# Optimization experiments

Hardware: AMD Instinct MI355X
Metric: run time of the kernel (lower is better)

Reference implementation:

```python
import jax, jax.numpy as jnp
import numpy as np

B, S, H, L, NH, FF, V, NL = 16, 512, 768, 12, 12, 3072, 30522, 9
DH = H // NH


def setup_inputs() -> dict:
    key = jax.random.key(0)
    ks = iter(jax.random.split(key, 16))
    def w(shape, scale=0.02):
        return jax.random.normal(next(ks), shape, jnp.float32) * scale
    return {
        "input_word_ids": jax.random.randint(next(ks), (B, S), 0, V, jnp.int32),
        "input_mask": jnp.ones((B, S), jnp.int32),
        "input_type_ids": jnp.zeros((B, S), jnp.int32),
        "valid_mask": jax.random.randint(next(ks), (B, S), 0, 2, jnp.int32),
        "word_emb": w((V, H)),
        "pos_emb": w((S, H)),
        "type_emb": w((2, H)),
        "emb_ln_g": jnp.ones((H,), jnp.float32),
        "emb_ln_b": jnp.zeros((H,), jnp.float32),
        "Wq": w((L, H, H)), "bq": jnp.zeros((L, H), jnp.float32),
        "Wk": w((L, H, H)), "bk": jnp.zeros((L, H), jnp.float32),
        "Wv": w((L, H, H)), "bv": jnp.zeros((L, H), jnp.float32),
        "Wo": w((L, H, H)), "bo": jnp.zeros((L, H), jnp.float32),
        "ln1_g": jnp.ones((L, H), jnp.float32), "ln1_b": jnp.zeros((L, H), jnp.float32),
        "W1": w((L, H, FF)), "b1": jnp.zeros((L, FF), jnp.float32),
        "W2": w((L, FF, H)), "b2": jnp.zeros((L, H), jnp.float32),
        "ln2_g": jnp.ones((L, H), jnp.float32), "ln2_b": jnp.zeros((L, H), jnp.float32),
        "cls_W": w((H, NL)), "cls_b": jnp.zeros((NL,), jnp.float32),
    }


def _layer_norm(x, g, b):
    m = x.mean(-1, keepdims=True)
    v = ((x - m) ** 2).mean(-1, keepdims=True)
    return (x - m) * jax.lax.rsqrt(v + 1e-12) * g + b


def reference(input_word_ids, input_mask, input_type_ids, valid_mask,
              word_emb, pos_emb, type_emb, emb_ln_g, emb_ln_b,
              Wq, bq, Wk, bk, Wv, bv, Wo, bo, ln1_g, ln1_b,
              W1, b1, W2, b2, ln2_g, ln2_b, cls_W, cls_b):
    b, s = input_word_ids.shape
    # --- BERT embeddings ---
    x = word_emb[input_word_ids] + pos_emb[None, :s] + type_emb[input_type_ids]
    x = _layer_norm(x, emb_ln_g, emb_ln_b)  # [B,S,H]
    attn_bias = (1.0 - input_mask.astype(jnp.float32))[:, None, None, :] * -1e9
    scale = 1.0 / np.sqrt(DH).astype(np.float32)

    def step(h, p):
        wq, bq_, wk, bk_, wv, bv_, wo, bo_, g1, gb1, w1, wb1, w2, wb2, g2, gb2 = p
        q = (h @ wq + bq_).reshape(b, s, NH, DH)
        k = (h @ wk + bk_).reshape(b, s, NH, DH)
        v = (h @ wv + bv_).reshape(b, s, NH, DH)
        scores = jnp.einsum('bqhd,bkhd->bhqk', q, k) * scale + attn_bias
        probs = jax.nn.softmax(scores, axis=-1)
        ctx = jnp.einsum('bhqk,bkhd->bqhd', probs, v).reshape(b, s, H)
        h = _layer_norm(h + ctx @ wo + bo_, g1, gb1)
        ff = jax.nn.gelu(h @ w1 + wb1, approximate=False)
        h = _layer_norm(h + ff @ w2 + wb2, g2, gb2)
        return h, None

    params = (Wq, bq, Wk, bk, Wv, bv, Wo, bo, ln1_g, ln1_b, W1, b1, W2, b2, ln2_g, ln2_b)
    x, _ = jax.lax.scan(step, x, params)

    # --- valid-token compaction (vectorized form of the python double loop) ---
    # valid tokens packed to the front (stable order), remainder zero-padded
    invalid = (1 - valid_mask).astype(jnp.int32)
    perm = jnp.argsort(invalid, axis=1, stable=True)          # [B,S]
    compact = jnp.take_along_axis(x, perm[:, :, None], axis=1)
    counts = valid_mask.sum(axis=1)                           # [B]
    keep = (jnp.arange(s)[None, :] < counts[:, None])[:, :, None]
    compact = jnp.where(keep, compact, jnp.zeros((), x.dtype))
    # dropout is identity at inference (training=False)
    logits = jax.nn.softmax(compact @ cls_W + cls_b, axis=-1)  # [B,S,NL]
    return logits
```

## Files before the change

### kernel.cpp

```cpp
#include <hip/hip_runtime.h>
#include <cstdint>
#include <cstddef>

#define B_ 16
#define S_ 512
#define H_ 768
#define L_ 12
#define NH_ 12
#define DH_ 64
#define FF_ 3072
#define NL_ 9

typedef _Float16 f16x8 __attribute__((ext_vector_type(8)));
typedef float f32x4 __attribute__((ext_vector_type(4)));

__device__ __forceinline__ float block_sum256(float v, float* red) {
#pragma unroll
  for (int off = 32; off; off >>= 1) v += __shfl_down(v, off);
  __syncthreads();
  if ((threadIdx.x & 63) == 0) red[threadIdx.x >> 6] = v;
  __syncthreads();
  return red[0] + red[1] + red[2] + red[3];
}

__device__ __forceinline__ float gelu_f(float x) {
  return 0.5f * x * (1.0f + erff(x * 0.70710678118654752f));
}

__global__ __launch_bounds__(256) void embed_ln_kernel(
    const int* __restrict__ wid, const int* __restrict__ tpid,
    const float* __restrict__ we, const float* __restrict__ pe,
    const float* __restrict__ te, const float* __restrict__ g,
    const float* __restrict__ bb, float* __restrict__ h,
    _Float16* __restrict__ hb) {
  __shared__ float red[4];
  int tok = blockIdx.x;
  int s = tok & (S_ - 1);
  int w = wid[tok], tp = tpid[tok];
  int t = threadIdx.x;
  float x[3];
#pragma unroll
  for (int i = 0; i < 3; ++i) {
    int j = t + i * 256;
    x[i] = we[(size_t)w * H_ + j] + pe[(size_t)s * H_ + j] + te[(size_t)tp * H_ + j];
  }
  float m = block_sum256(x[0] + x[1] + x[2], red) * (1.0f / H_);
  float d0 = x[0] - m, d1 = x[1] - m, d2 = x[2] - m;
  float var = block_sum256(d0 * d0 + d1 * d1 + d2 * d2, red) * (1.0f / H_);
  float rs = rsqrtf(var + 1e-12f);
#pragma unroll
  for (int i = 0; i < 3; ++i) {
    int j = t + i * 256;
    float v = (x[i] - m) * rs * g[j] + bb[j];
    h[(size_t)tok * H_ + j] = v;
    hb[(size_t)tok * H_ + j] = (_Float16)v;
  }
}

__global__ __launch_bounds__(256) void add_ln_kernel(
    float* __restrict__ h, const float* __restrict__ delta,
    const float* __restrict__ g, const float* __restrict__ bb,
    _Float16* __restrict__ hb) {
  __shared__ float red[4];
  int tok = blockIdx.x;
  int t = threadIdx.x;
  float x[3];
#pragma unroll
  for (int i = 0; i < 3; ++i) {
    int j = t + i * 256;
    x[i] = h[(size_t)tok * H_ + j] + delta[(size_t)tok * H_ + j];
  }
  float m = block_sum256(x[0] + x[1] + x[2], red) * (1.0f / H_);
  float d0 = x[0] - m, d1 = x[1] - m, d2 = x[2] - m;
  float var = block_sum256(d0 * d0 + d1 * d1 + d2 * d2, red) * (1.0f / H_);
  float rs = rsqrtf(var + 1e-12f);
#pragma unroll
  for (int i = 0; i < 3; ++i) {
    int j = t + i * 256;
    float v = (x[i] - m) * rs * g[j] + bb[j];
    h[(size_t)tok * H_ + j] = v;
    hb[(size_t)tok * H_ + j] = (_Float16)v;
  }
}

__global__ __launch_bounds__(256) void convert_weights_kernel(
    const float* __restrict__ Wq, const float* __restrict__ Wk,
    const float* __restrict__ Wv, const float* __restrict__ Wo,
    const float* __restrict__ W1, const float* __restrict__ W2,
    _Float16* __restrict__ qT, _Float16* __restrict__ kT,
    _Float16* __restrict__ vT, _Float16* __restrict__ oT,
    _Float16* __restrict__ w1T, _Float16* __restrict__ w2T) {
  __shared__ float T[64][65];
  int id = blockIdx.x;
  const float* src;
  _Float16* dst;
  int K, N, tk, tn;
  if (id < 576) {
    int mat = id / 144, t = id % 144;
    K = 768; N = 768; tk = t / 12; tn = t % 12;
    src = (mat == 0) ? Wq : (mat == 1) ? Wk : (mat == 2) ? Wv : Wo;
    dst = (mat == 0) ? qT : (mat == 1) ? kT : (mat == 2) ? vT : oT;
  } else if (id < 1152) {
    int t = id - 576; K = 768; N = 3072; tk = t / 48; tn = t % 48;
    src = W1; dst = w1T;
  } else {
    int t = id - 1152; K = 3072; N = 768; tk = t / 12; tn = t % 12;
    src = W2; dst = w2T;
  }
  int tid = threadIdx.x;
  int k0 = tk * 64, n0 = tn * 64;
  {
    int r = tid >> 4, c4 = (tid & 15) * 4;
#pragma unroll
    for (int i = 0; i < 4; ++i) {
      float4 v = *(const float4*)&src[(size_t)(k0 + r + i * 16) * N + n0 + c4];
      T[r + i * 16][c4 + 0] = v.x;
      T[r + i * 16][c4 + 1] = v.y;
      T[r + i * 16][c4 + 2] = v.z;
      T[r + i * 16][c4 + 3] = v.w;
    }
  }
  __syncthreads();
#pragma unroll
  for (int i = 0; i < 2; ++i) {
    int chunk = tid + i * 256;
    int n = chunk >> 3, kc = (chunk & 7) * 8;
    f16x8 o;
#pragma unroll
    for (int j = 0; j < 8; ++j) o[j] = (_Float16)T[kc + j][n];
    *(f16x8*)&dst[(size_t)(n0 + n) * K + k0 + kc] = o;
  }
}

template <int OUT>
__global__ __launch_bounds__(256) void gemm_f16(
    const _Float16* __restrict__ A, const _Float16* __restrict__ Bt,
    const float* __restrict__ bias, void* __restrict__ Cv,
    int M, int N, int K) {
  __shared__ _Float16 As[128 * 40];
  __shared__ _Float16 Bs[128 * 40];
  int tid = threadIdx.x;
  int lane = tid & 63, w = tid >> 6;
  int wr = w >> 1, wc = w & 1;
  int row0 = blockIdx.y * 128, col0 = blockIdx.x * 128;
  int l15 = lane & 15, kb = lane >> 4;

  int sr = tid >> 2, sc = tid & 3;
  const f16x8* ag0 = (const f16x8*)&A[(size_t)(row0 + sr) * K + sc * 8];
  const f16x8* ag1 = (const f16x8*)&A[(size_t)(row0 + 64 + sr) * K + sc * 8];
  const f16x8* bg0 = (const f16x8*)&Bt[(size_t)(col0 + sr) * K + sc * 8];
  const f16x8* bg1 = (const f16x8*)&Bt[(size_t)(col0 + 64 + sr) * K + sc * 8];
  f16x8* aw0 = (f16x8*)&As[sr * 40 + sc * 8];
  f16x8* aw1 = (f16x8*)&As[(64 + sr) * 40 + sc * 8];
  f16x8* bw0 = (f16x8*)&Bs[sr * 40 + sc * 8];
  f16x8* bw1 = (f16x8*)&Bs[(64 + sr) * 40 + sc * 8];

  f32x4 acc[4][4] = {};
  f16x8 ra0 = ag0[0], ra1 = ag1[0], rb0 = bg0[0], rb1 = bg1[0];
  int nk = K >> 5;
  for (int kt = 0; kt < nk; ++kt) {
    __syncthreads();
    *aw0 = ra0; *aw1 = ra1; *bw0 = rb0; *bw1 = rb1;
    __syncthreads();
    if (kt + 1 < nk) {
      int off = (kt + 1) * 4;
      ra0 = ag0[off]; ra1 = ag1[off]; rb0 = bg0[off]; rb1 = bg1[off];
    }
    f16x8 af[4], bf[4];
#pragma unroll
    for (int m = 0; m < 4; ++m)
      af[m] = *(const f16x8*)&As[(wr * 64 + m * 16 + l15) * 40 + kb * 8];
#pragma unroll
    for (int n = 0; n < 4; ++n)
      bf[n] = *(const f16x8*)&Bs[(wc * 64 + n * 16 + l15) * 40 + kb * 8];
#pragma unroll
    for (int m = 0; m < 4; ++m)
#pragma unroll
      for (int n = 0; n < 4; ++n)
        acc[m][n] = __builtin_amdgcn_mfma_f32_16x16x32_f16(af[m], bf[n], acc[m][n], 0, 0, 0);
  }
#pragma unroll
  for (int n = 0; n < 4; ++n) {
    int col = col0 + wc * 64 + n * 16 + l15;
    float bv = bias[col];
#pragma unroll
    for (int m = 0; m < 4; ++m) {
      int rowb = row0 + wr * 64 + m * 16 + kb * 4;
#pragma unroll
      for (int r = 0; r < 4; ++r) {
        float v = acc[m][n][r] + bv;
        if (OUT == 2) v = gelu_f(v);
        if (OUT == 0)
          ((float*)Cv)[(size_t)(rowb + r) * N + col] = v;
        else
          ((_Float16*)Cv)[(size_t)(rowb + r) * N + col] = (_Float16)v;
      }
    }
  }
}

__global__ __launch_bounds__(256) void vtrans_kernel(
    const _Float16* __restrict__ vb, _Float16* __restrict__ vt) {
  __shared__ _Float16 T[64][72];
  int s0 = blockIdx.x * 64;
  int bh = blockIdx.y;
  int b = bh / NH_, h = bh % NH_;
  int tid = threadIdx.x;
#pragma unroll
  for (int i = 0; i < 2; ++i) {
    int chunk = tid + i * 256;
    int s = chunk >> 3, dc = (chunk & 7) * 8;
    *(f16x8*)&T[s][dc] = *(const f16x8*)&vb[(size_t)(b * S_ + s0 + s) * H_ + h * DH_ + dc];
  }
  __syncthreads();
#pragma unroll
  for (int i = 0; i < 2; ++i) {
    int chunk = tid + i * 256;
    int d = chunk >> 3, sc = (chunk & 7) * 8;
    f16x8 o;
#pragma unroll
    for (int j = 0; j < 8; ++j) o[j] = T[sc + j][d];
    *(f16x8*)&vt[(size_t)(bh * DH_ + d) * S_ + s0 + sc] = o;
  }
}

__global__ __launch_bounds__(256) void flash_attn_kernel(
    const _Float16* __restrict__ q, const _Float16* __restrict__ k,
    const _Float16* __restrict__ vt, const int* __restrict__ mask,
    _Float16* __restrict__ ctx) {
  __shared__ _Float16 Ks[128 * 72];
  __shared__ _Float16 Vs[64 * 136];
  __shared__ _Float16 Ps[4][16 * 136];
  __shared__ float biasz[S_];
  int qt = blockIdx.x, h = blockIdx.y, b = blockIdx.z;
  int tid = threadIdx.x, lane = tid & 63, w = tid >> 6;
  int l15 = lane & 15, kb = lane >> 4;
  const float C = 0.125f * 1.44269504088896f;

  for (int i = tid; i < S_; i += 256)
    biasz[i] = (1.0f - (float)mask[b * S_ + i]) * (-1e9f * C);

  int qrow = b * S_ + qt * 64 + w * 16 + l15;
  f16x8 qf[2];
  qf[0] = *(const f16x8*)&q[(size_t)qrow * H_ + h * DH_ + kb * 8];
  qf[1] = *(const f16x8*)&q[(size_t)qrow * H_ + h * DH_ + 32 + kb * 8];

  auto loadKV = [&](int kt, f16x8* rk, f16x8* rv) {
#pragma unroll
    for (int i = 0; i < 4; ++i) {
      int idx = tid + i * 256;
      int r = idx >> 3, c = idx & 7;
      rk[i] = *(const f16x8*)&k[(size_t)(b * S_ + kt * 128 + r) * H_ + h * DH_ + c * 8];
      int d = idx >> 4, c2 = idx & 15;
      rv[i] = *(const f16x8*)&vt[(size_t)((b * NH_ + h) * DH_ + d) * S_ + kt * 128 + c2 * 8];
    }
  };

  float m_run[4], l_run[4];
  f32x4 o[4] = {};
#pragma unroll
  for (int r = 0; r < 4; ++r) { m_run[r] = -1e30f; l_run[r] = 0.f; }

  f16x8 rk[4], rv[4];
  loadKV(0, rk, rv);
  for (int kt = 0; kt < 4; ++kt) {
    __syncthreads();
#pragma unroll
    for (int i = 0; i < 4; ++i) {
      int idx = tid + i * 256;
      int r = idx >> 3, c = idx & 7;
      *(f16x8*)&Ks[r * 72 + c * 8] = rk[i];
      int d = idx >> 4, c2 = idx & 15;
      *(f16x8*)&Vs[d * 136 + c2 * 8] = rv[i];
    }
    __syncthreads();
    if (kt < 3) loadKV(kt + 1, rk, rv);
    f32x4 s[8];
#pragma unroll
    for (int nf = 0; nf < 8; ++nf) {
      f16x8 b0 = *(const f16x8*)&Ks[(nf * 16 + l15) * 72 + kb * 8];
      f16x8 b1 = *(const f16x8*)&Ks[(nf * 16 + l15) * 72 + 32 + kb * 8];
      f32x4 z = {};
      z = __builtin_amdgcn_mfma_f32_16x16x32_f16(qf[0], b0, z, 0, 0, 0);
      z = __builtin_amdgcn_mfma_f32_16x16x32_f16(qf[1], b1, z, 0, 0, 0);
      s[nf] = z;
    }
    float zb[8];
#pragma unroll
    for (int nf = 0; nf < 8; ++nf) zb[nf] = biasz[kt * 128 + nf * 16 + l15];
    float pw[8][4];
    float corr[4];
#pragma unroll
    for (int r = 0; r < 4; ++r) {
      float mx = -1e30f;
#pragma unroll
      for (int nf = 0; nf < 8; ++nf) mx = fmaxf(mx, s[nf][r] * C + zb[nf]);
#pragma unroll
      for (int d = 1; d < 16; d <<= 1) mx = fmaxf(mx, __shfl_xor(mx, d));
      float mnew = fmaxf(m_run[r], mx);
      float cr = exp2f(m_run[r] - mnew);
      m_run[r] = mnew;
      corr[r] = cr;
      float sum = 0.f;
#pragma unroll
      for (int nf = 0; nf < 8; ++nf) {
        float pv = exp2f(s[nf][r] * C + zb[nf] - mnew);
        pw[nf][r] = pv;
        sum += pv;
      }
#pragma unroll
      for (int d = 1; d < 16; d <<= 1) sum += __shfl_xor(sum, d);
      l_run[r] = l_run[r] * cr + sum;
    }
#pragma unroll
    for (int nf2 = 0; nf2 < 4; ++nf2)
#pragma unroll
      for (int r = 0; r < 4; ++r) o[nf2][r] *= corr[r];
#pragma unroll
    for (int nf = 0; nf < 8; ++nf)
#pragma unroll
      for (int r = 0; r < 4; ++r)
        Ps[w][(kb * 4 + r) * 136 + nf * 16 + l15] = (_Float16)pw[nf][r];
#pragma unroll
    for (int ks = 0; ks < 4; ++ks) {
      f16x8 pa = *(const f16x8*)&Ps[w][l15 * 136 + ks * 32 + kb * 8];
#pragma unroll
      for (int nf2 = 0; nf2 < 4; ++nf2) {
        f16x8 vb2 = *(const f16x8*)&Vs[(nf2 * 16 + l15) * 136 + ks * 32 + kb * 8];
        o[nf2] = __builtin_amdgcn_mfma_f32_16x16x32_f16(pa, vb2, o[nf2], 0, 0, 0);
      }
    }
  }
  float inv[4];
#pragma unroll
  for (int r = 0; r < 4; ++r) inv[r] = 1.0f / fmaxf(l_run[r], 1e-37f);
#pragma unroll
  for (int nf2 = 0; nf2 < 4; ++nf2)
#pragma unroll
    for (int r = 0; r < 4; ++r) {
      int row = b * S_ + qt * 64 + w * 16 + kb * 4 + r;
      ctx[(size_t)row * H_ + h * DH_ + nf2 * 16 + l15] = (_Float16)(o[nf2][r] * inv[r]);
    }
}

__global__ void compact_idx_kernel(const int* __restrict__ valid, int* __restrict__ dest) {
  int b = threadIdx.x;
  if (b >= B_) return;
  int cnt = 0;
  for (int s = 0; s < S_; ++s) {
    int vv = valid[b * S_ + s];
    dest[b * S_ + s] = vv ? cnt : -1;
    cnt += vv;
  }
}

__global__ __launch_bounds__(256) void scatter_kernel(
    const float* __restrict__ h, const int* __restrict__ dest,
    float* __restrict__ compact) {
  int tok = blockIdx.x;
  int d = dest[tok];
  if (d < 0) return;
  int b = tok >> 9;
  size_t src = (size_t)tok * H_;
  size_t dst = ((size_t)(b * S_ + d)) * H_;
  for (int j = threadIdx.x; j < H_; j += 256) compact[dst + j] = h[src + j];
}

__global__ __launch_bounds__(256) void cls_kernel(
    const float* __restrict__ x, const float* __restrict__ W,
    const float* __restrict__ bias2, float* __restrict__ out) {
  int lane = threadIdx.x & 63, wv = threadIdx.x >> 6;
  int tok = blockIdx.x * 4 + wv;
  float acc[NL_] = {};
  for (int hh = lane; hh < H_; hh += 64) {
    float xv = x[(size_t)tok * H_ + hh];
#pragma unroll
    for (int n = 0; n < NL_; ++n) acc[n] = fmaf(xv, W[hh * NL_ + n], acc[n]);
  }
#pragma unroll
  for (int n = 0; n < NL_; ++n) {
#pragma unroll
    for (int off = 32; off; off >>= 1) acc[n] += __shfl_down(acc[n], off);
  }
  if (lane == 0) {
    float vls[NL_], mx = -1e30f;
#pragma unroll
    for (int n = 0; n < NL_; ++n) {
      vls[n] = acc[n] + bias2[n];
      mx = fmaxf(mx, vls[n]);
    }
    float s = 0.f;
#pragma unroll
    for (int n = 0; n < NL_; ++n) {
      vls[n] = expf(vls[n] - mx);
      s += vls[n];
    }
    float inv = 1.0f / s;
#pragma unroll
    for (int n = 0; n < NL_; ++n) out[(size_t)tok * NL_ + n] = vls[n] * inv;
  }
}

extern "C" void kernel_launch(void* const* d_in, const int* in_sizes, int n_in,
                              void* d_out, int out_size, void* d_ws, size_t ws_size,
                              hipStream_t stream) {
  const int* wid = (const int*)d_in[0];
  const int* mask = (const int*)d_in[1];
  const int* tpid = (const int*)d_in[2];
  const int* valid = (const int*)d_in[3];
  const float* we = (const float*)d_in[4];
  const float* pe = (const float*)d_in[5];
  const float* te = (const float*)d_in[6];
  const float* eg = (const float*)d_in[7];
  const float* eb = (const float*)d_in[8];
  const float* Wq = (const float*)d_in[9];
  const float* bq = (const float*)d_in[10];
  const float* Wk = (const float*)d_in[11];
  const float* bk = (const float*)d_in[12];
  const float* Wv = (const float*)d_in[13];
  const float* bv = (const float*)d_in[14];
  const float* Wo = (const float*)d_in[15];
  const float* bo = (const float*)d_in[16];
  const float* g1 = (const float*)d_in[17];
  const float* gb1 = (const float*)d_in[18];
  const float* W1 = (const float*)d_in[19];
  const float* bf1 = (const float*)d_in[20];
  const float* W2 = (const float*)d_in[21];
  const float* bf2 = (const float*)d_in[22];
  const float* g2 = (const float*)d_in[23];
  const float* gb2 = (const float*)d_in[24];
  const float* cW = (const float*)d_in[25];
  const float* cb = (const float*)d_in[26];
  float* out = (float*)d_out;

  const size_t TOK = (size_t)B_ * S_;
  char* ws = (char*)d_ws;
  float* h = (float*)ws;
  _Float16* hb = (_Float16*)(ws + 25165824);
  float* t1 = (float*)(ws + 37748736);
  char* un1 = ws + 62914560;
  _Float16* qb = (_Float16*)un1;
  _Float16* kb = (_Float16*)(un1 + 12582912);
  _Float16* vb = (_Float16*)(un1 + 25165824);
  _Float16* vt = (_Float16*)(un1 + 37748736);
  _Float16* ffh = (_Float16*)un1;
  _Float16* ctx = (_Float16*)(ws + 113246208);
  char* wbuf = ws + 125829120;
  _Float16* wqT = (_Float16*)wbuf;
  _Float16* wkT = (_Float16*)(wbuf + 1179648);
  _Float16* wvT = (_Float16*)(wbuf + 2359296);
  _Float16* woT = (_Float16*)(wbuf + 3538944);
  _Float16* w1T = (_Float16*)(wbuf + 4718592);
  _Float16* w2T = (_Float16*)(wbuf + 9437184);
  int* dest = (int*)(ws + 139984896);

  dim3 blk(256);
  embed_ln_kernel<<<dim3((unsigned)TOK), blk, 0, stream>>>(wid, tpid, we, pe, te, eg, eb, h, hb);

  dim3 gH(H_ / 128, TOK / 128);
  dim3 gF(FF_ / 128, TOK / 128);
  for (int l = 0; l < L_; ++l) {
    convert_weights_kernel<<<dim3(1728), blk, 0, stream>>>(
        Wq + (size_t)l * H_ * H_, Wk + (size_t)l * H_ * H_,
        Wv + (size_t)l * H_ * H_, Wo + (size_t)l * H_ * H_,
        W1 + (size_t)l * H_ * FF_, W2 + (size_t)l * FF_ * H_,
        wqT, wkT, wvT, woT, w1T, w2T);
    gemm_f16<1><<<gH, blk, 0, stream>>>(hb, wqT, bq + l * H_, qb, (int)TOK, H_, H_);
    gemm_f16<1><<<gH, blk, 0, stream>>>(hb, wkT, bk + l * H_, kb, (int)TOK, H_, H_);
    gemm_f16<1><<<gH, blk, 0, stream>>>(hb, wvT, bv + l * H_, vb, (int)TOK, H_, H_);
    vtrans_kernel<<<dim3(S_ / 64, B_ * NH_), blk, 0, stream>>>(vb, vt);
    flash_attn_kernel<<<dim3(S_ / 64, NH_, B_), blk, 0, stream>>>(qb, kb, vt, mask, ctx);
    gemm_f16<0><<<gH, blk, 0, stream>>>(ctx, woT, bo + l * H_, t1, (int)TOK, H_, H_);
    add_ln_kernel<<<dim3((unsigned)TOK), blk, 0, stream>>>(h, t1, g1 + l * H_, gb1 + l * H_, hb);
    gemm_f16<2><<<gF, blk, 0, stream>>>(hb, w1T, bf1 + l * FF_, ffh, (int)TOK, FF_, H_);
    gemm_f16<0><<<gH, blk, 0, stream>>>(ffh, w2T, bf2 + l * H_, t1, (int)TOK, H_, FF_);
    add_ln_kernel<<<dim3((unsigned)TOK), blk, 0, stream>>>(h, t1, g2 + l * H_, gb2 + l * H_, hb);
  }

  compact_idx_kernel<<<1, 64, 0, stream>>>(valid, dest);
  hipMemsetAsync(t1, 0, TOK * H_ * sizeof(float), stream);
  scatter_kernel<<<dim3((unsigned)TOK), blk, 0, stream>>>(h, dest, t1);
  cls_kernel<<<dim3((unsigned)(TOK / 4)), blk, 0, stream>>>(t1, cW, cb, out);
}
```

Baseline: 4.042 ms.

## Fuse QKV projections into one GEMM and use direct global-to-LDS loads

The three separate Q, K and V projection GEMMs become one GEMM with N=2304 over the contiguous transposed weights. A small kernel concatenates the three biases, and attention and the V-transpose now read the interleaved QKV buffer through a row-stride parameter. Separately, the GEMM tile loads now use global_load_lds to write straight into unpadded LDS instead of going through a register prefetch. This removes extra launches and register traffic, but it drops the overlap of the next tile's load with the MFMA work and removes the LDS padding, which may cause bank conflicts on fragment reads.

```diff
diff --git a/kernel.cpp b/kernel.cpp
--- a/kernel.cpp
+++ b/kernel.cpp
@@ -10,9 +10,16 @@
 #define DH_ 64
 #define FF_ 3072
 #define NL_ 9
+#define QKV_ 2304
 
 typedef _Float16 f16x8 __attribute__((ext_vector_type(8)));
 typedef float f32x4 __attribute__((ext_vector_type(4)));
+
+__device__ __forceinline__ void load_lds16(const void* g, void* l) {
+  __builtin_amdgcn_global_load_lds(
+      (const __attribute__((address_space(1))) unsigned int*)g,
+      (__attribute__((address_space(3))) unsigned int*)l, 16, 0, 0);
+}
 
 __device__ __forceinline__ float block_sum256(float v, float* red) {
 #pragma unroll
@@ -132,47 +139,56 @@
   }
 }
 
+__global__ void biascat_kernel(const float* __restrict__ bq, const float* __restrict__ bk,
+                               const float* __restrict__ bv, float* __restrict__ o) {
+  int t = threadIdx.x;
+  for (int j = t; j < H_; j += 256) {
+    o[j] = bq[j];
+    o[H_ + j] = bk[j];
+    o[2 * H_ + j] = bv[j];
+  }
+}
+
 template <int OUT>
 __global__ __launch_bounds__(256) void gemm_f16(
     const _Float16* __restrict__ A, const _Float16* __restrict__ Bt,
     const float* __restrict__ bias, void* __restrict__ Cv,
     int M, int N, int K) {
-  __shared__ _Float16 As[128 * 40];
-  __shared__ _Float16 Bs[128 * 40];
+  __shared__ _Float16 As[128 * 32];
+  __shared__ _Float16 Bs[128 * 32];
   int tid = threadIdx.x;
   int lane = tid & 63, w = tid >> 6;
   int wr = w >> 1, wc = w & 1;
   int row0 = blockIdx.y * 128, col0 = blockIdx.x * 128;
   int l15 = lane & 15, kb = lane >> 4;
 
-  int sr = tid >> 2, sc = tid & 3;
-  const f16x8* ag0 = (const f16x8*)&A[(size_t)(row0 + sr) * K + sc * 8];
-  const f16x8* ag1 = (const f16x8*)&A[(size_t)(row0 + 64 + sr) * K + sc * 8];
-  const f16x8* bg0 = (const f16x8*)&Bt[(size_t)(col0 + sr) * K + sc * 8];
-  const f16x8* bg1 = (const f16x8*)&Bt[(size_t)(col0 + 64 + sr) * K + sc * 8];
-  f16x8* aw0 = (f16x8*)&As[sr * 40 + sc * 8];
-  f16x8* aw1 = (f16x8*)&As[(64 + sr) * 40 + sc * 8];
-  f16x8* bw0 = (f16x8*)&Bs[sr * 40 + sc * 8];
-  f16x8* bw1 = (f16x8*)&Bs[(64 + sr) * 40 + sc * 8];
+  int srow = lane >> 2, scol = (lane & 3) * 8;
+  const _Float16* gA0 = A + (size_t)(row0 + (w * 2 + 0) * 16 + srow) * K + scol;
+  const _Float16* gA1 = A + (size_t)(row0 + (w * 2 + 1) * 16 + srow) * K + scol;
+  const _Float16* gB0 = Bt + (size_t)(col0 + (w * 2 + 0) * 16 + srow) * K + scol;
+  const _Float16* gB1 = Bt + (size_t)(col0 + (w * 2 + 1) * 16 + srow) * K + scol;
+  char* lA0 = (char*)As + (w * 2 + 0) * 1024;
+  char* lA1 = (char*)As + (w * 2 + 1) * 1024;
+  char* lB0 = (char*)Bs + (w * 2 + 0) * 1024;
+  char* lB1 = (char*)Bs + (w * 2 + 1) * 1024;
 
   f32x4 acc[4][4] = {};
-  f16x8 ra0 = ag0[0], ra1 = ag1[0], rb0 = bg0[0], rb1 = bg1[0];
   int nk = K >> 5;
   for (int kt = 0; kt < nk; ++kt) {
+    int ko = kt * 32;
     __syncthreads();
-    *aw0 = ra0; *aw1 = ra1; *bw0 = rb0; *bw1 = rb1;
+    load_lds16(gA0 + ko, lA0);
+    load_lds16(gA1 + ko, lA1);
+    load_lds16(gB0 + ko, lB0);
+    load_lds16(gB1 + ko, lB1);
     __syncthreads();
-    if (kt + 1 < nk) {
-      int off = (kt + 1) * 4;
-      ra0 = ag0[off]; ra1 = ag1[off]; rb0 = bg0[off]; rb1 = bg1[off];
-    }
     f16x8 af[4], bf[4];
 #pragma unroll
     for (int m = 0; m < 4; ++m)
-      af[m] = *(const f16x8*)&As[(wr * 64 + m * 16 + l15) * 40 + kb * 8];
+      af[m] = *(const f16x8*)&As[(wr * 64 + m * 16 + l15) * 32 + kb * 8];
 #pragma unroll
     for (int n = 0; n < 4; ++n)
-      bf[n] = *(const f16x8*)&Bs[(wc * 64 + n * 16 + l15) * 40 + kb * 8];
+      bf[n] = *(const f16x8*)&Bs[(wc * 64 + n * 16 + l15) * 32 + kb * 8];
 #pragma unroll
     for (int m = 0; m < 4; ++m)
 #pragma unroll
@@ -200,7 +216,7 @@
 }
 
 __global__ __launch_bounds__(256) void vtrans_kernel(
-    const _Float16* __restrict__ vb, _Float16* __restrict__ vt) {
+    const _Float16* __restrict__ v, int RS, _Float16* __restrict__ vt) {
   __shared__ _Float16 T[64][72];
   int s0 = blockIdx.x * 64;
   int bh = blockIdx.y;
@@ -210,7 +226,7 @@
   for (int i = 0; i < 2; ++i) {
     int chunk = tid + i * 256;
     int s = chunk >> 3, dc = (chunk & 7) * 8;
-    *(f16x8*)&T[s][dc] = *(const f16x8*)&vb[(size_t)(b * S_ + s0 + s) * H_ + h * DH_ + dc];
+    *(f16x8*)&T[s][dc] = *(const f16x8*)&v[(size_t)(b * S_ + s0 + s) * RS + h * DH_ + dc];
   }
   __syncthreads();
 #pragma unroll
@@ -226,7 +242,7 @@
 
 __global__ __launch_bounds__(256) void flash_attn_kernel(
     const _Float16* __restrict__ q, const _Float16* __restrict__ k,
-    const _Float16* __restrict__ vt, const int* __restrict__ mask,
+    const _Float16* __restrict__ vt, int RS, const int* __restrict__ mask,
     _Float16* __restrict__ ctx) {
   __shared__ _Float16 Ks[128 * 72];
   __shared__ _Float16 Vs[64 * 136];
@@ -242,15 +258,15 @@
 
   int qrow = b * S_ + qt * 64 + w * 16 + l15;
   f16x8 qf[2];
-  qf[0] = *(const f16x8*)&q[(size_t)qrow * H_ + h * DH_ + kb * 8];
-  qf[1] = *(const f16x8*)&q[(size_t)qrow * H_ + h * DH_ + 32 + kb * 8];
+  qf[0] = *(const f16x8*)&q[(size_t)qrow * RS + h * DH_ + kb * 8];
+  qf[1] = *(const f16x8*)&q[(size_t)qrow * RS + h * DH_ + 32 + kb * 8];
 
   auto loadKV = [&](int kt, f16x8* rk, f16x8* rv) {
 #pragma unroll
     for (int i = 0; i < 4; ++i) {
       int idx = tid + i * 256;
       int r = idx >> 3, c = idx & 7;
-      rk[i] = *(const f16x8*)&k[(size_t)(b * S_ + kt * 128 + r) * H_ + h * DH_ + c * 8];
+      rk[i] = *(const f16x8*)&k[(size_t)(b * S_ + kt * 128 + r) * RS + h * DH_ + c * 8];
       int d = idx >> 4, c2 = idx & 15;
       rv[i] = *(const f16x8*)&vt[(size_t)((b * NH_ + h) * DH_ + d) * S_ + kt * 128 + c2 * 8];
     }
@@ -439,9 +455,7 @@
   _Float16* hb = (_Float16*)(ws + 25165824);
   float* t1 = (float*)(ws + 37748736);
   char* un1 = ws + 62914560;
-  _Float16* qb = (_Float16*)un1;
-  _Float16* kb = (_Float16*)(un1 + 12582912);
-  _Float16* vb = (_Float16*)(un1 + 25165824);
+  _Float16* qkv = (_Float16*)un1;
   _Float16* vt = (_Float16*)(un1 + 37748736);
   _Float16* ffh = (_Float16*)un1;
   _Float16* ctx = (_Float16*)(ws + 113246208);
@@ -453,10 +467,12 @@
   _Float16* w1T = (_Float16*)(wbuf + 4718592);
   _Float16* w2T = (_Float16*)(wbuf + 9437184);
   int* dest = (int*)(ws + 139984896);
+  float* qkvb = (float*)(ws + 140017664);
 
   dim3 blk(256);
   embed_ln_kernel<<<dim3((unsigned)TOK), blk, 0, stream>>>(wid, tpid, we, pe, te, eg, eb, h, hb);
 
+  dim3 gQKV(QKV_ / 128, TOK / 128);
   dim3 gH(H_ / 128, TOK / 128);
   dim3 gF(FF_ / 128, TOK / 128);
   for (int l = 0; l < L_; ++l) {
@@ -465,11 +481,11 @@
         Wv + (size_t)l * H_ * H_, Wo + (size_t)l * H_ * H_,
         W1 + (size_t)l * H_ * FF_, W2 + (size_t)l * FF_ * H_,
         wqT, wkT, wvT, woT, w1T, w2T);
-    gemm_f16<1><<<gH, blk, 0, stream>>>(hb, wqT, bq + l * H_, qb, (int)TOK, H_, H_);
-    gemm_f16<1><<<gH, blk, 0, stream>>>(hb, wkT, bk + l * H_, kb, (int)TOK, H_, H_);
-    gemm_f16<1><<<gH, blk, 0, stream>>>(hb, wvT, bv + l * H_, vb, (int)TOK, H_, H_);
-    vtrans_kernel<<<dim3(S_ / 64, B_ * NH_), blk, 0, stream>>>(vb, vt);
-    flash_attn_kernel<<<dim3(S_ / 64, NH_, B_), blk, 0, stream>>>(qb, kb, vt, mask, ctx);
+    biascat_kernel<<<dim3(1), blk, 0, stream>>>(bq + l * H_, bk + l * H_, bv + l * H_, qkvb);
+    gemm_f16<1><<<gQKV, blk, 0, stream>>>(hb, wqT, qkvb, qkv, (int)TOK, QKV_, H_);
+    vtrans_kernel<<<dim3(S_ / 64, B_ * NH_), blk, 0, stream>>>(qkv + 2 * H_, QKV_, vt);
+    flash_attn_kernel<<<dim3(S_ / 64, NH_, B_), blk, 0, stream>>>(
+        qkv, qkv + H_, vt, QKV_, mask, ctx);
     gemm_f16<0><<<gH, blk, 0, stream>>>(ctx, woT, bo + l * H_, t1, (int)TOK, H_, H_);
     add_ln_kernel<<<dim3((unsigned)TOK), blk, 0, stream>>>(h, t1, g1 + l * H_, gb1 + l * H_, hb);
     gemm_f16<2><<<gF, blk, 0, stream>>>(hb, w1T, bf1 + l * FF_, ffh, (int)TOK, FF_, H_);
```

Measured after the change: 4.107 ms. No clear change (+1.6%).
